# Optimization experiments

Measured on AMD Instinct MI355X. Metric: run time of the kernel, lower is better.

Reference implementation:

```python
import jax, jax.numpy as jnp
import numpy as np

B, D, H = 16, 512, 8
MA, MR = 2048, 256  # padded max atoms / residues per graph
EPS = 1e-5


def _counts():
    ca = 1024 + (np.arange(B) * 97) % 1024   # atoms per graph
    cr = 128 + (np.arange(B) * 37) % 128     # residues per graph
    return ca, cr


def to_dense(x, batch, M):
    """PyG to_dense_batch: flat [N, D] + sorted batch ids -> [B, M, D] padded + mask."""
    N = x.shape[0]
    counts = jax.ops.segment_sum(jnp.ones(N, jnp.int32), batch, num_segments=B)
    starts = jnp.concatenate([jnp.zeros(1, counts.dtype), jnp.cumsum(counts)[:-1]])
    pos = jnp.arange(N, dtype=jnp.int32) - starts[batch]
    dense = jnp.zeros((B, M, x.shape[1]), x.dtype).at[batch, pos].set(x)
    mask = jnp.zeros((B, M), bool).at[batch, pos].set(True)
    return dense, mask, batch, pos


def mha(q, k, v, in_w, in_b, out_w, out_b, key_valid):
    """torch nn.MultiheadAttention (batch_first, eval) with key_padding_mask = ~key_valid."""
    Lq, Lk = q.shape[1], k.shape[1]
    dh = D // H
    wq, wk, wv = in_w[:D], in_w[D:2 * D], in_w[2 * D:]
    bq, bk, bv = in_b[:D], in_b[D:2 * D], in_b[2 * D:]
    qh = (q @ wq.T + bq).reshape(B, Lq, H, dh)
    kh = (k @ wk.T + bk).reshape(B, Lk, H, dh)
    vh = (v @ wv.T + bv).reshape(B, Lk, H, dh)
    scores = jnp.einsum('bqhd,bkhd->bhqk', qh, kh) / jnp.sqrt(jnp.asarray(dh, q.dtype))
    scores = jnp.where(key_valid[:, None, None, :], scores, jnp.asarray(-1e9, scores.dtype))
    attn = jax.nn.softmax(scores, axis=-1)
    out = jnp.einsum('bhqk,bkhd->bqhd', attn, vh).reshape(B, Lq, D)
    return out @ out_w.T + out_b


def layernorm(x, g, b):
    m = x.mean(-1, keepdims=True)
    v = ((x - m) ** 2).mean(-1, keepdims=True)
    return (x - m) * jax.lax.rsqrt(v + EPS) * g + b


def setup_inputs() -> dict:
    key = jax.random.key(0)
    ks = jax.random.split(key, 8)
    ca, cr = _counts()
    Na, Nr = int(ca.sum()), int(cr.sum())
    s = 0.02
    return {
        'atom_node': jax.random.normal(ks[0], (Na, D), jnp.float32),
        'res_node': jax.random.normal(ks[1], (Nr, D), jnp.float32),
        'r2a_in_w': jax.random.normal(ks[2], (3 * D, D), jnp.float32) * s,
        'r2a_in_b': jnp.zeros((3 * D,), jnp.float32),
        'r2a_out_w': jax.random.normal(ks[3], (D, D), jnp.float32) * s,
        'r2a_out_b': jnp.zeros((D,), jnp.float32),
        'a2r_in_w': jax.random.normal(ks[4], (3 * D, D), jnp.float32) * s,
        'a2r_in_b': jnp.zeros((3 * D,), jnp.float32),
        'a2r_out_w': jax.random.normal(ks[5], (D, D), jnp.float32) * s,
        'a2r_out_b': jnp.zeros((D,), jnp.float32),
        'atom_ln_g': jnp.ones((D,), jnp.float32),
        'atom_ln_b': jnp.zeros((D,), jnp.float32),
        'res_ln_g': jnp.ones((D,), jnp.float32),
        'res_ln_b': jnp.zeros((D,), jnp.float32),
        'atom_batch': jnp.asarray(np.repeat(np.arange(B), ca), jnp.int32),
        'res_batch': jnp.asarray(np.repeat(np.arange(B), cr), jnp.int32),
    }


def reference(atom_node, res_node, r2a_in_w, r2a_in_b, r2a_out_w, r2a_out_b,
              a2r_in_w, a2r_in_b, a2r_out_w, a2r_out_b,
              atom_ln_g, atom_ln_b, res_ln_g, res_ln_b,
              atom_batch, res_batch):
    atom_d, atom_mask, ab, ap = to_dense(atom_node, atom_batch, MA)
    res_d, res_mask, rb, rp = to_dense(res_node, res_batch, MR)
    # res2atom: atoms attend over residues; atom2res: residues attend over (updated) atoms
    atom_upd = mha(atom_d, res_d, res_d, r2a_in_w, r2a_in_b, r2a_out_w, r2a_out_b, res_mask)
    res_upd = mha(res_d, atom_upd, atom_upd, a2r_in_w, a2r_in_b, a2r_out_w, a2r_out_b, atom_mask)
    atom_out = layernorm(atom_upd, atom_ln_g, atom_ln_b)[ab, ap] + atom_node
    res_out = layernorm(res_upd, res_ln_g, res_ln_b)[rb, rp] + res_node
    return atom_out, res_out
```

## Files before the change

### kernel.cpp

```cpp
#include <hip/hip_runtime.h>
#include <hip/hip_bf16.h>
#include <math.h>

#define DD 512
#define NA_TOT 22904
#define NR_TOT 2904
#define MPAD_A 22960
#define MPAD_R 2960

__constant__ int c_aoff[17] = {0,1024,2145,3363,4678,6090,7599,9205,10908,12708,
                               14605,16599,17666,18830,20091,21449,22904};
__constant__ int c_roff[17] = {0,128,293,495,734,882,1067,1289,1420,1588,
                               1793,2035,2186,2374,2599,2733,2904};
__constant__ int c_apad[17] = {0,1024,2152,3376,4696,6112,7624,9232,10936,12736,
                               14640,16640,17712,18880,20144,21504,22960};
__constant__ int c_rpad[17] = {0,128,296,504,744,896,1088,1312,1448,1616,
                               1824,2072,2224,2416,2648,2784,2960};

typedef __attribute__((ext_vector_type(8))) short short8;
typedef __attribute__((ext_vector_type(4))) float f32x4;
typedef __attribute__((ext_vector_type(4))) unsigned short ushort4v;

__device__ __forceinline__ unsigned short f2bf(float f) {
  __hip_bfloat16 h = __float2bfloat16(f);
  return *reinterpret_cast<unsigned short*>(&h);
}
__device__ __forceinline__ float bf2f(unsigned short u) {
  union { unsigned int i; float f; } c; c.i = ((unsigned int)u) << 16; return c.f;
}
__device__ __forceinline__ float wred_sum(float x){
#pragma unroll
  for (int o = 32; o > 0; o >>= 1) x += __shfl_xor(x, o, 64);
  return x;
}

__device__ __forceinline__ void gl_lds16(const unsigned short* g, unsigned short* l) {
  __builtin_amdgcn_global_load_lds(
      (const __attribute__((address_space(1))) unsigned int*)g,
      (__attribute__((address_space(3))) unsigned int*)l, 16, 0, 0);
}

__global__ __launch_bounds__(256) void cvt5(
    const float* __restrict__ s0, const float* __restrict__ s1,
    const float* __restrict__ s2, const float* __restrict__ s3,
    const float* __restrict__ s4,
    unsigned short* __restrict__ d0, unsigned short* __restrict__ d1,
    unsigned short* __restrict__ d2, unsigned short* __restrict__ d3,
    unsigned short* __restrict__ d4,
    int n0, int n1, int n2, int n3, int n4)
{
  const float* s; unsigned short* d; int n;
  switch (blockIdx.y) {
    case 0: s = s0; d = d0; n = n0; break;
    case 1: s = s1; d = d1; n = n1; break;
    case 2: s = s2; d = d2; n = n2; break;
    case 3: s = s3; d = d3; n = n3; break;
    default: s = s4; d = d4; n = n4; break;
  }
  const int i = (blockIdx.x * 256 + threadIdx.x) * 4;
  if (i < n) {
    const float4 v = *reinterpret_cast<const float4*>(s + i);
    ushort4v o = { f2bf(v.x), f2bf(v.y), f2bf(v.z), f2bf(v.w) };
    *reinterpret_cast<ushort4v*>(d + i) = o;
  }
}

__global__ __launch_bounds__(256) void mkmap(int* __restrict__ mapA,
                                             int* __restrict__ mapR)
{
  const int pm = blockIdx.x * 256 + threadIdx.x;
  if (pm < MPAD_A) {
    int b = 0;
#pragma unroll
    for (int i = 1; i < 16; ++i) if (pm >= c_apad[i]) b = i;
    const int rel = pm - c_apad[b];
    const int L = c_aoff[b+1] - c_aoff[b];
    mapA[pm] = c_aoff[b] + min(rel, L - 1);
  }
  if (pm < MPAD_R) {
    int b = 0;
#pragma unroll
    for (int i = 1; i < 16; ++i) if (pm >= c_rpad[i]) b = i;
    const int rel = pm - c_rpad[b];
    const int L = c_roff[b+1] - c_roff[b];
    mapR[pm] = c_roff[b] + min(rel, L - 1);
  }
}

struct GSeg {
  const void* X; const unsigned short* W; const float* bias;
  unsigned short* Y; const int* map;
  int M; int ldY; int mtiles; int flags;
};
struct GSeg4 { GSeg s[4]; };

__global__ __launch_bounds__(256) void gemm_multi(GSeg4 P, int mtpx)
{
  __shared__ unsigned short SMEM[4*128*64];
  unsigned short* const X0 = SMEM;
  unsigned short* const W0 = SMEM + 8192;
  unsigned short* const X1 = SMEM + 16384;
  unsigned short* const W1 = SMEM + 24576;
  const GSeg sg = P.s[blockIdx.y];
  const int xcd = blockIdx.x & 7, g = blockIdx.x >> 3;
  const int mt = xcd + 8 * (g % mtpx);
  const int nt = g / mtpx;
  if (mt >= sg.mtiles) return;
  const int m0 = mt * 128, n0 = nt * 128;
  const int INF32 = sg.flags & 1, OUTT = sg.flags & 2, REMAP = sg.flags & 4;
  const int tid = threadIdx.x, lane = tid & 63, w = tid >> 6;
  const int la = lane & 15, lg = lane >> 4;
  const int wm = (w & 1) * 64, wn = (w >> 1) * 64;
  const int w64 = w * 64;

  f32x4 acc[4][4];
#pragma unroll
  for (int i = 0; i < 4; ++i)
#pragma unroll
    for (int j = 0; j < 4; ++j) acc[i][j] = (f32x4){0.f,0.f,0.f,0.f};

  int elA[4][2], elB[4][2];
#pragma unroll
  for (int i = 0; i < 4; ++i)
#pragma unroll
    for (int kc = 0; kc < 2; ++kc) {
      { const int r = wm + i*16 + la;
        elA[i][kc] = r*64 + ((kc*32 + lg*8) ^ ((r & 7) << 3)); }
      { const int r = wn + i*16 + la;
        elB[i][kc] = r*64 + ((kc*32 + lg*8) ^ ((r & 7) << 3)); }
    }

  int srow[4];
#pragma unroll
  for (int p = 0; p < 4; ++p) {
    const int slot = p*256 + tid;
    const int rg = min(m0 + (slot >> 3), sg.M - 1);
    srow[p] = REMAP ? sg.map[rg] : rg;
  }
  int scg[4], srw[4];
#pragma unroll
  for (int p = 0; p < 4; ++p) {
    const int slot = p*256 + tid;
    srw[p] = slot >> 3;
    scg[p] = ((slot & 7) ^ (srw[p] & 7)) << 3;
  }

  float4 xr[4][2];

#define STAGE_W(DST, kb_)                                                       \
  _Pragma("unroll")                                                             \
  for (int p = 0; p < 4; ++p)                                                   \
    gl_lds16(sg.W + (size_t)(n0 + srw[p]) * DD + (kb_) + scg[p],                \
             &(DST)[(p*256 + w64) * 8]);

#define STAGE_XB(DST, kb_)                                                      \
  _Pragma("unroll")                                                             \
  for (int p = 0; p < 4; ++p)                                                   \
    gl_lds16((const unsigned short*)sg.X + (size_t)srow[p] * DD + (kb_) + scg[p],\
             &(DST)[(p*256 + w64) * 8]);

#define LOAD_XF(kb_)                                                            \
  _Pragma("unroll")                                                             \
  for (int p = 0; p < 4; ++p) {                                                 \
    const float* src = (const float*)sg.X + (size_t)srow[p] * DD + (kb_) + scg[p];\
    xr[p][0] = *reinterpret_cast<const float4*>(src);                           \
    xr[p][1] = *reinterpret_cast<const float4*>(src + 4);                       \
  }

#define WRITE_XF(DST)                                                           \
  _Pragma("unroll")                                                             \
  for (int p = 0; p < 4; ++p) {                                                 \
    short8 pk;                                                                  \
    pk[0] = (short)f2bf(xr[p][0].x); pk[1] = (short)f2bf(xr[p][0].y);           \
    pk[2] = (short)f2bf(xr[p][0].z); pk[3] = (short)f2bf(xr[p][0].w);           \
    pk[4] = (short)f2bf(xr[p][1].x); pk[5] = (short)f2bf(xr[p][1].y);           \
    pk[6] = (short)f2bf(xr[p][1].z); pk[7] = (short)f2bf(xr[p][1].w);           \
    *reinterpret_cast<short8*>(&(DST)[(p*256 + tid) * 8]) = pk;                 \
  }

#define COMPUTE(XB, WB)                                                         \
  {                                                                             \
    short8 af[4][2], bfm[4][2];                                                 \
    _Pragma("unroll")                                                           \
    for (int i = 0; i < 4; ++i)                                                 \
      _Pragma("unroll")                                                         \
      for (int kc = 0; kc < 2; ++kc) {                                          \
        af[i][kc]  = *reinterpret_cast<const short8*>(&(XB)[elA[i][kc]]);       \
        bfm[i][kc] = *reinterpret_cast<const short8*>(&(WB)[elB[i][kc]]);       \
      }                                                                         \
    _Pragma("unroll")                                                           \
    for (int kc = 0; kc < 2; ++kc)                                              \
      _Pragma("unroll")                                                         \
      for (int i = 0; i < 4; ++i)                                               \
        _Pragma("unroll")                                                       \
        for (int j = 0; j < 4; ++j)                                             \
          acc[i][j] = __builtin_amdgcn_mfma_f32_16x16x32_bf16(af[i][kc], bfm[j][kc], acc[i][j], 0, 0, 0); \
  }

  if (INF32) { LOAD_XF(0); WRITE_XF(X0); }
  else       { STAGE_XB(X0, 0); }
  STAGE_W(W0, 0);
  __syncthreads();

#pragma unroll
  for (int t = 0; t < 4; ++t) {
    const int kb1 = t*128 + 64;
    if (INF32) { LOAD_XF(kb1); } else { STAGE_XB(X1, kb1); }
    STAGE_W(W1, kb1);
    COMPUTE(X0, W0);
    if (INF32) { WRITE_XF(X1); }
    __syncthreads();
    const int kb2 = t*128 + 128;
    if (kb2 < DD) {
      if (INF32) { LOAD_XF(kb2); } else { STAGE_XB(X0, kb2); }
      STAGE_W(W0, kb2);
    }
    COMPUTE(X1, W1);
    if (INF32 && kb2 < DD) { WRITE_XF(X0); }
    __syncthreads();
  }

#undef STAGE_W
#undef STAGE_XB
#undef LOAD_XF
#undef WRITE_XF
#undef COMPUTE

  unsigned short* Cs = SMEM;
  if (!OUTT) {
#pragma unroll
    for (int j = 0; j < 4; ++j) {
      const int n = wn + j*16 + la;
      const float bj = sg.bias[n0 + n];
#pragma unroll
      for (int i = 0; i < 4; ++i) {
        const int mb = wm + i*16 + lg*4;
#pragma unroll
        for (int r = 0; r < 4; ++r) {
          const int m = mb + r;
          Cs[m*128 + (((n >> 3) ^ (m & 7)) << 3) + (n & 7)] = f2bf(acc[i][j][r] + bj);
        }
      }
    }
    __syncthreads();
#pragma unroll
    for (int p = 0; p < 8; ++p) {
      const int sid = p*256 + tid;
      const int row = sid >> 4, s = sid & 15;
      if (m0 + row < sg.M) {
        const short8 v = *reinterpret_cast<const short8*>(&Cs[row*128 + ((s ^ (row & 7)) << 3)]);
        *reinterpret_cast<short8*>(sg.Y + (size_t)(m0 + row)*sg.ldY + n0 + s*8) = v;
      }
    }
  } else {
#pragma unroll
    for (int j = 0; j < 4; ++j) {
      const int n = wn + j*16 + la;
      const float bj = sg.bias[n0 + n];
#pragma unroll
      for (int i = 0; i < 4; ++i) {
        const int mb = wm + i*16 + lg*4;
#pragma unroll
        for (int r = 0; r < 4; ++r) {
          const int m = mb + r;
          Cs[n*128 + (((m >> 3) ^ (n & 7)) << 3) + (m & 7)] = f2bf(acc[i][j][r] + bj);
        }
      }
    }
    __syncthreads();
#pragma unroll
    for (int p = 0; p < 8; ++p) {
      const int sid = p*256 + tid;
      const int row = sid >> 4, s = sid & 15;
      if (m0 + s*8 < sg.M) {
        const short8 v = *reinterpret_cast<const short8*>(&Cs[row*128 + ((s ^ (row & 7)) << 3)]);
        *reinterpret_cast<short8*>(sg.Y + (size_t)(n0 + row)*sg.ldY + m0 + s*8) = v;
      }
    }
  }
}

template<int SWAP>
__global__ __launch_bounds__(256, 4) void attn_v7(const unsigned short* __restrict__ Q,
                                                  const unsigned short* __restrict__ K,
                                                  const unsigned short* __restrict__ VT,
                                                  unsigned short* __restrict__ O, int ldvt)
{
  __shared__ unsigned short Ks[2][64*64];
  __shared__ unsigned short Vs[2][64*64];
  __shared__ unsigned short Pl[4][16*64];
  const int* qo  = SWAP ? c_roff : c_aoff;
  const int* ko  = SWAP ? c_aoff : c_roff;
  const int* kop = SWAP ? c_apad : c_rpad;
  const int b = blockIdx.x >> 3, h = blockIdx.x & 7;
  const int Lq = qo[b+1]-qo[b], Lk = ko[b+1]-ko[b];
  const int padL = kop[b+1]-kop[b];
  const int q0b = blockIdx.y * 64;
  if (q0b >= Lq) return;
  const int tid = threadIdx.x, w = tid >> 6, lane = tid & 63;
  const int la = lane & 15, lg = lane >> 4;
  const int q0 = q0b + w*16;
  const unsigned short* Qb  = Q  + (size_t)qo[b]*DD + h*64;
  const unsigned short* Kb  = K  + (size_t)kop[b]*DD + h*64;
  const unsigned short* VTb = VT + (size_t)(h*64)*ldvt + kop[b];

  short8 qf[2];
  {
    const int qrow = min(q0 + la, Lq - 1);
    qf[0] = *reinterpret_cast<const short8*>(Qb + (size_t)qrow*DD + lg*8);
    qf[1] = *reinterpret_cast<const short8*>(Qb + (size_t)qrow*DD + 32 + lg*8);
  }

  f32x4 acc[4];
#pragma unroll
  for (int j = 0; j < 4; ++j) acc[j] = (f32x4){0.f,0.f,0.f,0.f};
  float lsum[4] = {0.f,0.f,0.f,0.f};

  const int nkc = (Lk + 63) >> 6;

#define STAGE(bi, kc_)                                                          \
  {                                                                             \
    const int kbase_ = (kc_) * 64;                                              \
    _Pragma("unroll")                                                           \
    for (int p = 0; p < 2; ++p) {                                               \
      const int slot = p*256 + tid;                                             \
      const int row = slot >> 3, cg = slot & 7;                                 \
      const int srow = min(kbase_ + row, padL - 1);                             \
      gl_lds16(Kb + (size_t)srow * DD + ((cg ^ (row & 7)) << 3),                \
               &Ks[bi][(p*256 + w*64) * 8]);                                    \
    }                                                                           \
    _Pragma("unroll")                                                           \
    for (int p = 0; p < 2; ++p) {                                               \
      const int slot = p*256 + tid;                                             \
      const int row = slot >> 3, cg = slot & 7;                                 \
      const int col = min(kbase_ + ((cg ^ (row & 7)) << 3), padL - 8);          \
      gl_lds16(VTb + (size_t)row * ldvt + col, &Vs[bi][(p*256 + w*64) * 8]);    \
    }                                                                           \
  }

  STAGE(0, 0);
  __syncthreads();

  for (int kc = 0; kc < nkc; ++kc) {
    const int bi = kc & 1;
    if (kc + 1 < nkc) STAGE(bi ^ 1, kc + 1);
    const int kbase = kc * 64;

    f32x4 S[4];
#pragma unroll
    for (int j = 0; j < 4; ++j) {
      const int row = j*16 + la;
      const short8 kf0 = *reinterpret_cast<const short8*>(
          &Ks[bi][row*64 + ((lg*8) ^ ((row & 7) << 3))]);
      const short8 kf1 = *reinterpret_cast<const short8*>(
          &Ks[bi][row*64 + ((32 + lg*8) ^ ((row & 7) << 3))]);
      f32x4 s = (f32x4){0.f,0.f,0.f,0.f};
      s = __builtin_amdgcn_mfma_f32_16x16x32_bf16(qf[0], kf0, s, 0, 0, 0);
      s = __builtin_amdgcn_mfma_f32_16x16x32_bf16(qf[1], kf1, s, 0, 0, 0);
      S[j] = s;
    }

#pragma unroll
    for (int j = 0; j < 4; ++j) {
      const bool ok = (kbase + j*16 + la) < Lk;
#pragma unroll
      for (int r = 0; r < 4; ++r) {
        const float p = ok ? __expf(S[j][r] * 0.125f) : 0.f;
        S[j][r] = p;
        lsum[r] += p;
      }
    }

#pragma unroll
    for (int r = 0; r < 4; ++r) {
      const int prow = lg*4 + r;
#pragma unroll
      for (int j = 0; j < 4; ++j)
        Pl[w][prow*64 + ((j*16 + la) ^ ((prow & 7) << 3))] = f2bf(S[j][r]);
    }
    __builtin_amdgcn_wave_barrier();
    const short8 pf0 = *reinterpret_cast<const short8*>(
        &Pl[w][la*64 + ((lg*8) ^ ((la & 7) << 3))]);
    const short8 pf1 = *reinterpret_cast<const short8*>(
        &Pl[w][la*64 + ((32 + lg*8) ^ ((la & 7) << 3))]);

#pragma unroll
    for (int j = 0; j < 4; ++j) {
      const int d = j*16 + la;
      const short8 vf0 = *reinterpret_cast<const short8*>(
          &Vs[bi][d*64 + ((lg*8) ^ ((d & 7) << 3))]);
      const short8 vf1 = *reinterpret_cast<const short8*>(
          &Vs[bi][d*64 + ((32 + lg*8) ^ ((d & 7) << 3))]);
      acc[j] = __builtin_amdgcn_mfma_f32_16x16x32_bf16(pf0, vf0, acc[j], 0, 0, 0);
      acc[j] = __builtin_amdgcn_mfma_f32_16x16x32_bf16(pf1, vf1, acc[j], 0, 0, 0);
    }
    __syncthreads();
  }

#pragma unroll
  for (int msk = 1; msk <= 8; msk <<= 1)
#pragma unroll
    for (int r = 0; r < 4; ++r) lsum[r] += __shfl_xor(lsum[r], msk, 64);

#pragma unroll
  for (int r = 0; r < 4; ++r) {
    const float inv = 1.f / lsum[r];
    const int prow = lg*4 + r;
#pragma unroll
    for (int j = 0; j < 4; ++j)
      Pl[w][prow*64 + ((j*16 + la) ^ ((prow & 7) << 3))] = f2bf(acc[j][r] * inv);
  }
  __builtin_amdgcn_wave_barrier();
#pragma unroll
  for (int p = 0; p < 2; ++p) {
    const int sid = p*64 + lane;
    const int row = sid >> 3, s = sid & 7;
    const int qrow = q0 + row;
    if (qrow < Lq) {
      const short8 v = *reinterpret_cast<const short8*>(
          &Pl[w][row*64 + ((s ^ (row & 7)) << 3)]);
      *reinterpret_cast<short8*>(O + (size_t)(qo[b] + qrow)*DD + h*64 + s*8) = v;
    }
  }
#undef STAGE
}

__global__ __launch_bounds__(256) void ln_res(const unsigned short* __restrict__ Ub,
    float* __restrict__ Yout,
    const float* __restrict__ atom_node, const float* __restrict__ res_node,
    const float* __restrict__ ag, const float* __restrict__ ab,
    const float* __restrict__ rg, const float* __restrict__ rb)
{
  const int row = blockIdx.x * 4 + (threadIdx.x >> 6);
  const int lane = threadIdx.x & 63;
  if (row >= NA_TOT + NR_TOT) return;
  const float* g; const float* bb; const float* resid;
  if (row < NA_TOT) { g = ag; bb = ab; resid = atom_node + (size_t)row * DD; }
  else { g = rg; bb = rb; resid = res_node + (size_t)(row - NA_TOT) * DD; }
  const short8 xb = *reinterpret_cast<const short8*>(Ub + (size_t)row*DD + lane*8);
  float xv[8];
#pragma unroll
  for (int i = 0; i < 8; ++i) xv[i] = bf2f((unsigned short)xb[i]);
  float s = 0.f;
#pragma unroll
  for (int i = 0; i < 8; ++i) s += xv[i];
  s = wred_sum(s);
  const float mean = s * (1.f/512.f);
  float vs = 0.f;
#pragma unroll
  for (int i = 0; i < 8; ++i) { const float d = xv[i] - mean; vs = fmaf(d, d, vs); }
  vs = wred_sum(vs) * (1.f/512.f);
  const float inv = rsqrtf(vs + 1e-5f);
  const float4 g0 = *reinterpret_cast<const float4*>(g + lane*8);
  const float4 g1 = *reinterpret_cast<const float4*>(g + lane*8 + 4);
  const float4 b0 = *reinterpret_cast<const float4*>(bb + lane*8);
  const float4 b1 = *reinterpret_cast<const float4*>(bb + lane*8 + 4);
  const float4 r0 = *reinterpret_cast<const float4*>(resid + lane*8);
  const float4 r1 = *reinterpret_cast<const float4*>(resid + lane*8 + 4);
  float4 o0, o1;
  o0.x = (xv[0]-mean)*inv*g0.x + b0.x + r0.x;
  o0.y = (xv[1]-mean)*inv*g0.y + b0.y + r0.y;
  o0.z = (xv[2]-mean)*inv*g0.z + b0.z + r0.z;
  o0.w = (xv[3]-mean)*inv*g0.w + b0.w + r0.w;
  o1.x = (xv[4]-mean)*inv*g1.x + b1.x + r1.x;
  o1.y = (xv[5]-mean)*inv*g1.y + b1.y + r1.y;
  o1.z = (xv[6]-mean)*inv*g1.z + b1.z + r1.z;
  o1.w = (xv[7]-mean)*inv*g1.w + b1.w + r1.w;
  float* y = Yout + (size_t)row * DD + lane*8;
  *reinterpret_cast<float4*>(y)     = o0;
  *reinterpret_cast<float4*>(y + 4) = o1;
}

extern "C" void kernel_launch(void* const* d_in, const int* in_sizes, int n_in,
                              void* d_out, int out_size, void* d_ws, size_t ws_size,
                              hipStream_t stream) {
  (void)in_sizes; (void)n_in; (void)out_size; (void)ws_size;
  const float* atom_node = (const float*)d_in[0];
  const float* res_node  = (const float*)d_in[1];
  const float* r2a_in_w  = (const float*)d_in[2];
  const float* r2a_in_b  = (const float*)d_in[3];
  const float* r2a_out_w = (const float*)d_in[4];
  const float* r2a_out_b = (const float*)d_in[5];
  const float* a2r_in_w  = (const float*)d_in[6];
  const float* a2r_in_b  = (const float*)d_in[7];
  const float* a2r_out_w = (const float*)d_in[8];
  const float* a2r_out_b = (const float*)d_in[9];
  const float* atom_ln_g = (const float*)d_in[10];
  const float* atom_ln_b = (const float*)d_in[11];
  const float* res_ln_g  = (const float*)d_in[12];
  const float* res_ln_b  = (const float*)d_in[13];

  float* out = (float*)d_out;
  unsigned short* wsb = (unsigned short*)d_ws;
  const size_t NAD = (size_t)NA_TOT * DD;
  const size_t NRD = (size_t)NR_TOT * DD;
  const size_t PAD = (size_t)MPAD_A * DD;
  const size_t PRD = (size_t)MPAD_R * DD;
  unsigned short* slab1  = wsb;
  unsigned short* slab2  = wsb + PAD;
  unsigned short* updb   = wsb + 2*PAD;
  unsigned short* res_bf = wsb + 2*PAD + NAD + NRD;
  unsigned short* K1     = res_bf + NRD;
  unsigned short* V1T    = K1 + PRD;
  unsigned short* Q2     = V1T + PRD;
  unsigned short* O2     = Q2 + NRD;
  unsigned short* wbf    = O2 + NRD;
  unsigned short* w_r2a_in  = wbf;
  unsigned short* w_r2a_out = wbf +  786432;
  unsigned short* w_a2r_in  = wbf + 1048576;
  unsigned short* w_a2r_out = wbf + 1835008;
  int* mapA = (int*)(wbf + 2097152);
  int* mapR = mapA + MPAD_A;
  unsigned short* Q1  = slab1;
  unsigned short* O1  = slab2;
  unsigned short* K2  = slab1;
  unsigned short* V2T = slab2;

  const dim3 blk(256);

  mkmap<<<dim3((MPAD_A + 255)/256), blk, 0, stream>>>(mapA, mapR);
  cvt5<<<dim3(1452, 5), blk, 0, stream>>>(
      r2a_in_w, r2a_out_w, a2r_in_w, a2r_out_w, res_node,
      w_r2a_in, w_r2a_out, w_a2r_in, w_a2r_out, res_bf,
      786432, 262144, 786432, 262144, (int)NRD);

  {
    GSeg4 A;
    A.s[0] = { atom_node, w_r2a_in,          r2a_in_b,        Q1,  nullptr, NA_TOT, 512,    179, 1 };
    A.s[1] = { res_bf,    w_r2a_in + 262144, r2a_in_b + 512,  K1,  mapR,    MPAD_R, 512,    24,  4 };
    A.s[2] = { res_bf,    w_r2a_in + 524288, r2a_in_b + 1024, V1T, mapR,    MPAD_R, MPAD_R, 24,  6 };
    A.s[3] = { res_bf,    w_a2r_in,          a2r_in_b,        Q2,  nullptr, NR_TOT, 512,    23,  0 };
    gemm_multi<<<dim3(736, 4), blk, 0, stream>>>(A, 23);
  }
  attn_v7<0><<<dim3(128, 32), blk, 0, stream>>>(Q1, K1, V1T, O1, MPAD_R);
  {
    GSeg4 B;
    B.s[0] = { O1, w_r2a_out, r2a_out_b, updb, nullptr, NA_TOT, 512, 179, 0 };
    B.s[1] = B.s[0]; B.s[2] = B.s[0]; B.s[3] = B.s[0];
    gemm_multi<<<dim3(736, 1), blk, 0, stream>>>(B, 23);
  }
  {
    GSeg4 C;
    C.s[0] = { updb, w_a2r_in + 262144, a2r_in_b + 512,  K2,  mapA, MPAD_A, 512,    180, 4 };
    C.s[1] = { updb, w_a2r_in + 524288, a2r_in_b + 1024, V2T, mapA, MPAD_A, MPAD_A, 180, 6 };
    C.s[2] = C.s[0]; C.s[3] = C.s[0];
    gemm_multi<<<dim3(736, 2), blk, 0, stream>>>(C, 23);
  }
  attn_v7<1><<<dim3(128, 4), blk, 0, stream>>>(Q2, K2, V2T, O2, MPAD_A);
  {
    GSeg4 E;
    E.s[0] = { O2, w_a2r_out, a2r_out_b, updb + NAD, nullptr, NR_TOT, 512, 23, 0 };
    E.s[1] = E.s[0]; E.s[2] = E.s[0]; E.s[3] = E.s[0];
    gemm_multi<<<dim3(96, 1), blk, 0, stream>>>(E, 3);
  }
  ln_res<<<dim3((NA_TOT + NR_TOT + 3) / 4), blk, 0, stream>>>(
      updb, out, atom_node, res_node, atom_ln_g, atom_ln_b, res_ln_g, res_ln_b);
}
```

Measured before the change: 214.3 us.

## Pre-convert atom features to bf16 and deepen GEMM LDS pipeline with async staging

Adds a separate kernel that converts the fp32 atom features to bf16 up front. The first GEMM then stages them straight into LDS through the async global-to-LDS path, instead of loading fp32 into registers and converting in-loop. The GEMM main loop is restructured into an 8-step pipeline with triple-buffered X tiles and double-buffered W tiles, using explicit vmcnt waits and raw barriers so loads run further ahead of the MFMA compute. This costs an extra launch and an extra pass over the atom array, plus more LDS per block, which may lower occupancy.

```diff
diff --git a/kernel.cpp b/kernel.cpp
--- a/kernel.cpp
+++ b/kernel.cpp
@@ -65,6 +65,22 @@
   }
 }
 
+__global__ __launch_bounds__(256) void cvt_atom(const float* __restrict__ s,
+                                                unsigned short* __restrict__ d, int n)
+{
+  const int i = (blockIdx.x * 256 + threadIdx.x) * 8;
+  if (i < n) {
+    const float4 v0 = *reinterpret_cast<const float4*>(s + i);
+    const float4 v1 = *reinterpret_cast<const float4*>(s + i + 4);
+    short8 pk;
+    pk[0] = (short)f2bf(v0.x); pk[1] = (short)f2bf(v0.y);
+    pk[2] = (short)f2bf(v0.z); pk[3] = (short)f2bf(v0.w);
+    pk[4] = (short)f2bf(v1.x); pk[5] = (short)f2bf(v1.y);
+    pk[6] = (short)f2bf(v1.z); pk[7] = (short)f2bf(v1.w);
+    *reinterpret_cast<short8*>(d + i) = pk;
+  }
+}
+
 __global__ __launch_bounds__(256) void mkmap(int* __restrict__ mapA,
                                              int* __restrict__ mapR)
 {
@@ -96,22 +112,24 @@
 
 __global__ __launch_bounds__(256) void gemm_multi(GSeg4 P, int mtpx)
 {
-  __shared__ unsigned short SMEM[4*128*64];
-  unsigned short* const X0 = SMEM;
-  unsigned short* const W0 = SMEM + 8192;
-  unsigned short* const X1 = SMEM + 16384;
-  unsigned short* const W1 = SMEM + 24576;
+  __shared__ unsigned short SMEM[40960];
+  unsigned short* const Xb0 = SMEM;
+  unsigned short* const Xb1 = SMEM + 8192;
+  unsigned short* const Xb2 = SMEM + 16384;
+  unsigned short* const Wb0 = SMEM + 24576;
+  unsigned short* const Wb1 = SMEM + 32768;
   const GSeg sg = P.s[blockIdx.y];
   const int xcd = blockIdx.x & 7, g = blockIdx.x >> 3;
   const int mt = xcd + 8 * (g % mtpx);
   const int nt = g / mtpx;
   if (mt >= sg.mtiles) return;
   const int m0 = mt * 128, n0 = nt * 128;
-  const int INF32 = sg.flags & 1, OUTT = sg.flags & 2, REMAP = sg.flags & 4;
+  const int OUTT = sg.flags & 2, REMAP = sg.flags & 4;
   const int tid = threadIdx.x, lane = tid & 63, w = tid >> 6;
   const int la = lane & 15, lg = lane >> 4;
   const int wm = (w & 1) * 64, wn = (w >> 1) * 64;
   const int w64 = w * 64;
+  const unsigned short* Xg = (const unsigned short*)sg.X;
 
   f32x4 acc[4][4];
 #pragma unroll
@@ -145,38 +163,17 @@
     scg[p] = ((slot & 7) ^ (srw[p] & 7)) << 3;
   }
 
-  float4 xr[4][2];
-
 #define STAGE_W(DST, kb_)                                                       \
   _Pragma("unroll")                                                             \
   for (int p = 0; p < 4; ++p)                                                   \
     gl_lds16(sg.W + (size_t)(n0 + srw[p]) * DD + (kb_) + scg[p],                \
              &(DST)[(p*256 + w64) * 8]);
 
-#define STAGE_XB(DST, kb_)                                                      \
+#define STAGE_X(DST, kb_)                                                       \
   _Pragma("unroll")                                                             \
   for (int p = 0; p < 4; ++p)                                                   \
-    gl_lds16((const unsigned short*)sg.X + (size_t)srow[p] * DD + (kb_) + scg[p],\
+    gl_lds16(Xg + (size_t)srow[p] * DD + (kb_) + scg[p],                        \
              &(DST)[(p*256 + w64) * 8]);
-
-#define LOAD_XF(kb_)                                                            \
-  _Pragma("unroll")                                                             \
-  for (int p = 0; p < 4; ++p) {                                                 \
-    const float* src = (const float*)sg.X + (size_t)srow[p] * DD + (kb_) + scg[p];\
-    xr[p][0] = *reinterpret_cast<const float4*>(src);                           \
-    xr[p][1] = *reinterpret_cast<const float4*>(src + 4);                       \
-  }
-
-#define WRITE_XF(DST)                                                           \
-  _Pragma("unroll")                                                             \
-  for (int p = 0; p < 4; ++p) {                                                 \
-    short8 pk;                                                                  \
-    pk[0] = (short)f2bf(xr[p][0].x); pk[1] = (short)f2bf(xr[p][0].y);           \
-    pk[2] = (short)f2bf(xr[p][0].z); pk[3] = (short)f2bf(xr[p][0].w);           \
-    pk[4] = (short)f2bf(xr[p][1].x); pk[5] = (short)f2bf(xr[p][1].y);           \
-    pk[6] = (short)f2bf(xr[p][1].z); pk[7] = (short)f2bf(xr[p][1].w);           \
-    *reinterpret_cast<short8*>(&(DST)[(p*256 + tid) * 8]) = pk;                 \
-  }
 
 #define COMPUTE(XB, WB)                                                         \
   {                                                                             \
@@ -197,35 +194,38 @@
           acc[i][j] = __builtin_amdgcn_mfma_f32_16x16x32_bf16(af[i][kc], bfm[j][kc], acc[i][j], 0, 0, 0); \
   }
 
-  if (INF32) { LOAD_XF(0); WRITE_XF(X0); }
-  else       { STAGE_XB(X0, 0); }
-  STAGE_W(W0, 0);
+  STAGE_W(Wb0, 0);
+  STAGE_X(Xb0, 0);
+  STAGE_X(Xb1, 64);
+
+#pragma unroll
+  for (int k = 0; k < 8; ++k) {
+    __builtin_amdgcn_s_barrier();
+    asm volatile("" ::: "memory");
+    if (k + 1 < 8) {
+      if (((k+1) & 1) == 0) { STAGE_W(Wb0, (k+1)*64); } else { STAGE_W(Wb1, (k+1)*64); }
+    }
+    if (k + 2 < 8) {
+      if (((k+2) % 3) == 0) { STAGE_X(Xb0, (k+2)*64); }
+      else if (((k+2) % 3) == 1) { STAGE_X(Xb1, (k+2)*64); }
+      else { STAGE_X(Xb2, (k+2)*64); }
+    }
+    if (k < 6)       { asm volatile("s_waitcnt vmcnt(12)" ::: "memory"); }
+    else if (k == 6) { asm volatile("s_waitcnt vmcnt(8)" ::: "memory"); }
+    else             { asm volatile("s_waitcnt vmcnt(0)" ::: "memory"); }
+    __builtin_amdgcn_s_barrier();
+    asm volatile("" ::: "memory");
+    __builtin_amdgcn_sched_barrier(0);
+    if ((k % 3) == 0)      { if ((k & 1) == 0) COMPUTE(Xb0, Wb0) else COMPUTE(Xb0, Wb1) }
+    else if ((k % 3) == 1) { if ((k & 1) == 0) COMPUTE(Xb1, Wb0) else COMPUTE(Xb1, Wb1) }
+    else                   { if ((k & 1) == 0) COMPUTE(Xb2, Wb0) else COMPUTE(Xb2, Wb1) }
+  }
+
+#undef STAGE_W
+#undef STAGE_X
+#undef COMPUTE
+
   __syncthreads();
-
-#pragma unroll
-  for (int t = 0; t < 4; ++t) {
-    const int kb1 = t*128 + 64;
-    if (INF32) { LOAD_XF(kb1); } else { STAGE_XB(X1, kb1); }
-    STAGE_W(W1, kb1);
-    COMPUTE(X0, W0);
-    if (INF32) { WRITE_XF(X1); }
-    __syncthreads();
-    const int kb2 = t*128 + 128;
-    if (kb2 < DD) {
-      if (INF32) { LOAD_XF(kb2); } else { STAGE_XB(X0, kb2); }
-      STAGE_W(W0, kb2);
-    }
-    COMPUTE(X1, W1);
-    if (INF32 && kb2 < DD) { WRITE_XF(X0); }
-    __syncthreads();
-  }
-
-#undef STAGE_W
-#undef STAGE_XB
-#undef LOAD_XF
-#undef WRITE_XF
-#undef COMPUTE
-
   unsigned short* Cs = SMEM;
   if (!OUTT) {
 #pragma unroll
@@ -511,10 +511,11 @@
   unsigned short* w_a2r_out = wbf + 1835008;
   int* mapA = (int*)(wbf + 2097152);
   int* mapR = mapA + MPAD_A;
-  unsigned short* Q1  = slab1;
-  unsigned short* O1  = slab2;
-  unsigned short* K2  = slab1;
-  unsigned short* V2T = slab2;
+  unsigned short* Q1      = slab1;
+  unsigned short* atom_bf = slab2;
+  unsigned short* O1      = slab2;
+  unsigned short* K2      = slab1;
+  unsigned short* V2T     = slab2;
 
   const dim3 blk(256);
 
@@ -523,13 +524,14 @@
       r2a_in_w, r2a_out_w, a2r_in_w, a2r_out_w, res_node,
       w_r2a_in, w_r2a_out, w_a2r_in, w_a2r_out, res_bf,
       786432, 262144, 786432, 262144, (int)NRD);
+  cvt_atom<<<dim3((int)(NAD/2048)), blk, 0, stream>>>(atom_node, atom_bf, (int)NAD);
 
   {
     GSeg4 A;
-    A.s[0] = { atom_node, w_r2a_in,          r2a_in_b,        Q1,  nullptr, NA_TOT, 512,    179, 1 };
-    A.s[1] = { res_bf,    w_r2a_in + 262144, r2a_in_b + 512,  K1,  mapR,    MPAD_R, 512,    24,  4 };
-    A.s[2] = { res_bf,    w_r2a_in + 524288, r2a_in_b + 1024, V1T, mapR,    MPAD_R, MPAD_R, 24,  6 };
-    A.s[3] = { res_bf,    w_a2r_in,          a2r_in_b,        Q2,  nullptr, NR_TOT, 512,    23,  0 };
+    A.s[0] = { atom_bf, w_r2a_in,          r2a_in_b,        Q1,  nullptr, NA_TOT, 512,    179, 0 };
+    A.s[1] = { res_bf,  w_r2a_in + 262144, r2a_in_b + 512,  K1,  mapR,    MPAD_R, 512,    24,  4 };
+    A.s[2] = { res_bf,  w_r2a_in + 524288, r2a_in_b + 1024, V1T, mapR,    MPAD_R, MPAD_R, 24,  6 };
+    A.s[3] = { res_bf,  w_a2r_in,          a2r_in_b,        Q2,  nullptr, NR_TOT, 512,    23,  0 };
     gemm_multi<<<dim3(736, 4), blk, 0, stream>>>(A, 23);
   }
   attn_v7<0><<<dim3(128, 32), blk, 0, stream>>>(Q1, K1, V1T, O1, MPAD_R);
```

Result: no change. 213.7 us (-0.3%).
